# Optimization experiments

Hardware: AMD Instinct MI355X
Metric: run time of the kernel (lower is better)

Reference implementation:

```python
import jax, jax.numpy as jnp
import numpy as np

EPS = 1e-5


def reference(hidden_states, mu_x, W_x1, W_x2, x_bias, W_r, W_k, W_v, W_g,
              A_w, B_w, b_w, bonus, gn_weight, gn_bias, W_o):
    B, T, D = hidden_states.shape
    Hh = bonus.shape[0]
    x = hidden_states
    # token shift: delta = shifted(x) - x, shifted pads one zero row at t=0
    shifted = jnp.pad(x, ((0, 0), (1, 0), (0, 0)))[:, :T]
    delta = shifted - x
    # x_proj: LerpLinear(D -> 5*lr) -> tanh -> einsum with second weight viewed [D,5,lr]
    lr = W_x1.shape[0] // 5
    z = jnp.tanh((x + delta * mu_x) @ W_x1.T).reshape(B, T, 5, lr)
    mus = jnp.einsum('blnr,dnr->blnd', z, W_x2.reshape(D, 5, lr)) + x_bias  # [B,T,5,D]
    r_mu, w_mu, k_mu, v_mu, g_mu = (mus[:, :, i] for i in range(5))
    # DDLerpLinear projections: linear(x + delta * mu)
    r = (x + delta * r_mu) @ W_r.T                                 # [B,T,KD]
    w = jnp.tanh((x + delta * w_mu) @ A_w.T) @ B_w.T + b_w          # LoRA w/ tanh
    k = (x + delta * k_mu) @ W_k.T
    v = (x + delta * v_mu) @ W_v.T                                 # [B,T,VD]
    g = (x + delta * g_mu) @ W_g.T
    K = W_r.shape[0] // Hh
    V = W_v.shape[0] // Hh
    r = r.reshape(B, T, Hh, K)
    k = k.reshape(B, T, Hh, K)
    w = -jnp.exp(w.reshape(B, T, Hh, K))  # log-decay, in (-inf, 0)
    v = v.reshape(B, T, Hh, V)
    u = bonus                              # [Hh, K]

    def step(S, inp):
        q_t, k_t, v_t, w_t = inp           # [B,Hh,K],[B,Hh,K],[B,Hh,V],[B,Hh,K]
        kv = k_t[..., :, None] * v_t[..., None, :]                  # [B,Hh,K,V]
        o_t = jnp.einsum('bhk,bhkv->bhv', q_t, S + u[None, :, :, None] * kv)
        S = jnp.exp(w_t)[..., None] * S + kv
        return S, o_t

    S0 = jnp.zeros((B, Hh, K, V), dtype=x.dtype)
    xs = (jnp.swapaxes(r, 0, 1), jnp.swapaxes(k, 0, 1),
          jnp.swapaxes(v, 0, 1), jnp.swapaxes(w, 0, 1))
    _, o = jax.lax.scan(step, S0, xs)       # o: [T,B,Hh,V]
    o = jnp.swapaxes(o, 0, 1)               # [B,T,Hh,V]
    # GroupNorm(num_heads, value_dim): normalize each head's V channels per token
    mean = o.mean(-1, keepdims=True)
    var = o.var(-1, keepdims=True)
    o = (o - mean) / jnp.sqrt(var + EPS)
    o = o.reshape(B, T, Hh * V) * gn_weight + gn_bias
    o = o * jax.nn.silu(g)                  # swish gate
    return o @ W_o.T


def setup_inputs() -> dict:
    key = jax.random.key(0)
    ks = jax.random.split(key, 16)
    B, T, D = 8, 2048, 1024
    Hh, KD, VD, LR, GLR = 4, 512, 1024, 32, 64
    s = 0.02
    w = lambda k, shape: jax.random.normal(k, shape, jnp.float32) * s
    return {
        'hidden_states': jax.random.normal(ks[0], (B, T, D), jnp.float32),
        'mu_x': w(ks[1], (D,)),
        'W_x1': w(ks[2], (5 * LR, D)),
        'W_x2': w(ks[3], (D, 5 * LR)),
        'x_bias': jnp.zeros((5, D), jnp.float32),
        'W_r': w(ks[4], (KD, D)),
        'W_k': w(ks[5], (KD, D)),
        'W_v': w(ks[6], (VD, D)),
        'W_g': w(ks[7], (VD, D)),
        'A_w': w(ks[8], (GLR, D)),
        'B_w': w(ks[9], (KD, GLR)),
        'b_w': jnp.zeros((KD,), jnp.float32),
        'bonus': w(ks[10], (Hh, KD // Hh)),
        'gn_weight': jnp.ones((VD,), jnp.float32),
        'gn_bias': jnp.zeros((VD,), jnp.float32),
        'W_o': w(ks[11], (D, VD)),
    }
```

## Files before the change

kernel.cpp:

```cpp
#include <hip/hip_runtime.h>
#include <hip/hip_bf16.h>
#include <hip/hip_fp16.h>
#include <cstdint>


typedef _Float16 half8 __attribute__((ext_vector_type(8)));
typedef float f32x4 __attribute__((ext_vector_type(4)));

#define CL 256
#define NP (CL / 2)
#define NC 8

__device__ __forceinline__ float hbits2f(unsigned short us) {
    __half h; *reinterpret_cast<unsigned short*>(&h) = us; return __half2float(h);
}
__device__ __forceinline__ unsigned short f2h(float f) {
    __half h = __float2half(f);
    return *reinterpret_cast<unsigned short*>(&h);
}
__device__ __forceinline__ float2 up2(unsigned int u) {
    return make_float2(hbits2f((unsigned short)(u & 0xFFFF)),
                       hbits2f((unsigned short)(u >> 16)));
}
__device__ __forceinline__ void gload_lds16(const void* g, void* l) {
    __builtin_amdgcn_global_load_lds(
        (const __attribute__((address_space(1))) unsigned*)g,
        (__attribute__((address_space(3))) unsigned*)l, 16, 0, 0);
}

__global__ void cast16(const float* __restrict__ src, __half* __restrict__ dst, int n4)
{
    const int i = blockIdx.x * blockDim.x + threadIdx.x;
    if (i >= n4) return;
    const float4 f = *(const float4*)(src + (size_t)i * 4);
    ushort4 u;
    u.x = f2h(f.x); u.y = f2h(f.y); u.z = f2h(f.z); u.w = f2h(f.w);
    *(ushort4*)(dst + (size_t)i * 4) = u;
}

__global__ void k_xw_h(const float* __restrict__ X, const float* __restrict__ mu,
                       __half* __restrict__ XW, int M, int T)
{
    const size_t i4 = (size_t)blockIdx.x * blockDim.x + threadIdx.x;
    if (i4 >= (size_t)M * 256) return;
    const size_t idx = i4 * 4;
    const int m = (int)(idx >> 10);
    const int d = (int)(idx & 1023);
    const int t = m & (T - 1);
    const float4 xv = *(const float4*)(X + idx);
    const float4 m4 = *(const float4*)(mu + d);
    float4 xp = make_float4(0.f, 0.f, 0.f, 0.f);
    if (t > 0) xp = *(const float4*)(X + idx - 1024);
    ushort4 o;
    o.x = f2h(xv.x + (xp.x - xv.x) * m4.x);
    o.y = f2h(xv.y + (xp.y - xv.y) * m4.y);
    o.z = f2h(xv.z + (xp.z - xv.z) * m4.z);
    o.w = f2h(xv.w + (xp.w - xv.w) * m4.w);
    *(ushort4*)(XW + idx) = o;
}

__global__ __launch_bounds__(256) void gemm16(
    const __half* __restrict__ A, int lda,
    const __half* __restrict__ B, int ldb,
    void* __restrict__ Cv, int ldc,
    int M, int N, int K,
    const float* __restrict__ bias, int epi,
    const float* __restrict__ X, int T)
{
    __shared__ __align__(16) _Float16 As[128 * 32];
    __shared__ __align__(16) _Float16 Bs[128 * 32];

    const int tid = threadIdx.x;

    const int nwg = gridDim.x * gridDim.y;
    int p = blockIdx.y * gridDim.x + blockIdx.x;
    if (!(nwg & 7)) p = (p & 7) * (nwg >> 3) + (p >> 3);
    const int bx = p % gridDim.x, by = p / gridDim.x;

    const int m0 = by * 128;
    const int n0 = bx * 128;
    const int wave = tid >> 6, lane = tid & 63;
    const int wm = wave >> 1, wn = wave & 1;
    const int lr = lane & 15, lk = lane >> 4;

    const int srow = tid >> 2;
    const int scol = (tid & 3) * 8;
    const int arow0 = m0 + srow, arow1 = m0 + 64 + srow;
    int brow0 = n0 + srow;      if (brow0 >= N) brow0 = N - 1;
    int brow1 = n0 + 64 + srow; if (brow1 >= N) brow1 = N - 1;
    char* dA = (char*)As + tid * 16;
    char* dB = (char*)Bs + tid * 16;

    f32x4 acc[4][4] = {};

    for (int k0 = 0; k0 < K; k0 += 32) {
        const __half* gA0 = A + (size_t)arow0 * lda + k0 + scol;
        const __half* gA1 = A + (size_t)arow1 * lda + k0 + scol;
        const __half* gB0 = B + (size_t)brow0 * ldb + k0 + scol;
        const __half* gB1 = B + (size_t)brow1 * ldb + k0 + scol;
        __syncthreads();
        gload_lds16(gA0, dA);
        gload_lds16(gA1, dA + 4096);
        gload_lds16(gB0, dB);
        gload_lds16(gB1, dB + 4096);
        __syncthreads();

        half8 af[4], bf[4];
#pragma unroll
        for (int f = 0; f < 4; f++) {
            af[f] = *(const half8*)&As[(wm * 64 + f * 16 + lr) * 32 + lk * 8];
            bf[f] = *(const half8*)&Bs[(wn * 64 + f * 16 + lr) * 32 + lk * 8];
        }
#pragma unroll
        for (int fm = 0; fm < 4; fm++)
#pragma unroll
            for (int fn = 0; fn < 4; fn++)
                acc[fm][fn] = __builtin_amdgcn_mfma_f32_16x16x32_f16(
                    af[fm], bf[fn], acc[fm][fn], 0, 0, 0);
    }

#pragma unroll
    for (int fm = 0; fm < 4; fm++) {
#pragma unroll
        for (int fn = 0; fn < 4; fn++) {
#pragma unroll
            for (int j = 0; j < 4; j++) {
                const int gm = m0 + wm * 64 + fm * 16 + lk * 4 + j;
                const int gn = n0 + wn * 64 + fn * 16 + lr;
                if (gn >= N) continue;
                float a = acc[fm][fn][j];
                if (epi == 1) {
                    a = tanhf(a);
                    ((__half*)Cv)[(size_t)gm * ldc + gn] = __float2half(a);
                } else if (epi == 2) {
                    a += bias[gn];
                    const float xv = X[(size_t)gm * 1024 + gn];
                    float xp = 0.f;
                    if (gm & (T - 1)) xp = X[(size_t)(gm - 1) * 1024 + gn];
                    ((__half*)Cv)[(size_t)gm * ldc + gn] =
                        __float2half(xv + (xp - xv) * a);
                } else if (epi == 3) {
                    a += bias[gn];
                    ((__half*)Cv)[(size_t)gm * ldc + gn] = __float2half(a);
                } else if (epi == 4) {
                    ((float*)Cv)[(size_t)gm * ldc + gn] = a;
                } else {
                    ((__half*)Cv)[(size_t)gm * ldc + gn] = __float2half(a);
                }
            }
        }
    }
}

__global__ __launch_bounds__(256) void k_prep(
    const __half* __restrict__ R, const __half* __restrict__ Kk,
    const __half* __restrict__ W, const float* __restrict__ bonus,
    unsigned* __restrict__ Eu, float* __restrict__ RU, int T)
{
    const int tok = blockIdx.x;
    const int b = tok >> 11, t = tok & 2047;
    const int h = threadIdx.x >> 6, lane = threadIdx.x & 63;
    const size_t base = (size_t)tok * 512 + h * 128 + 2 * lane;
    const unsigned rr = *(const unsigned*)(R + base);
    const unsigned kk = *(const unsigned*)(Kk + base);
    const unsigned ww = *(const unsigned*)(W + base);
    const float2 rf = up2(rr), kf = up2(kk), wf = up2(ww);
    const float d0 = __expf(-__expf(wf.x));
    const float d1 = __expf(-__expf(wf.y));
    const float2 uf = *(const float2*)(bonus + h * 128 + 2 * lane);
    float ru = rf.x * uf.x * kf.x + rf.y * uf.y * kf.y;
#pragma unroll
    for (int off = 1; off < 64; off <<= 1) ru += __shfl_xor(ru, off);
    const int bh = b * 4 + h;
    unsigned* ep = Eu + (size_t)(bh * T + t) * 192;
    uint2 rkw;
    rkw.x = (rr & 0xFFFFu) | (kk << 16);
    rkw.y = (rr >> 16) | (kk & 0xFFFF0000u);
    *(uint2*)(ep + 2 * lane) = rkw;
    ep[128 + lane] = (unsigned)f2h(d0) | ((unsigned)f2h(d1) << 16);
    if (lane == 0) RU[(size_t)bh * T + t] = ru;
}

__global__ __launch_bounds__(128) void a_gen(
    const unsigned* __restrict__ Eu, __half* __restrict__ Ab,
    float* __restrict__ Abuf, int T)
{
    const int p = blockIdx.x;
    const int l = (p & 7) * 28 + (p >> 3);
    const int bh = l / 7, ci = l - bh * 7;
    const int c = ci + 1;
    const int k = threadIdx.x;
    const int t0 = c * CL;
    const unsigned* ep = Eu + (size_t)(bh * T + t0) * 192;
    __half* ap = Ab + ((size_t)bh * T + t0) * 128 + k;
    const int sel = (k & 1) * 16;
    float D = 1.f;
#pragma unroll 4
    for (int t = 0; t < CL; ++t) {
        const unsigned* e = ep + (size_t)t * 192;
        const unsigned rk = e[k];
        const unsigned dw = e[128 + (k >> 1)];
        const float r = hbits2f((unsigned short)(rk & 0xFFFF));
        const float d = hbits2f((unsigned short)((dw >> sel) & 0xFFFF));
        ap[(size_t)t * 128] = __float2half(r * D);
        D *= d;
    }
    if (c < NC - 1) Abuf[(size_t)(c * 32 + bh) * 128 + k] = D;
}

__global__ __launch_bounds__(256) void rwkv_scan(
    const uint4* __restrict__ E, const __half* __restrict__ V,
    const float* __restrict__ RU, __half* __restrict__ Cout,
    __half* __restrict__ O, int T)
{
    __shared__ uint4 sE[4][96];
    __shared__ uint4 sV[4][16];
    __shared__ float sRU[4][2];

    const int p = blockIdx.x;
    const int l = (p & 7) * 128 + (p >> 3);
    const int bh = l >> 5, c = (l >> 2) & 7, vq = l & 3;
    const int b = bh >> 2, h = bh & 3;
    const int tid = threadIdx.x;
    const int w = tid >> 6, lane = tid & 63;
    const int kg = tid & 15, vg = tid >> 4;
    const int t0 = c * CL;

    const uint4* Eg = E + (size_t)(bh * T + t0) * 48;
    const uint4* Vgp = (const uint4*)(V + ((size_t)b * T + t0) * 1024 + h * 256 + vq * 64);
    const float* RUp = RU + (size_t)bh * T + t0;
    __half* Op = O + ((size_t)b * T + t0) * 1024 + h * 256 + vq * 64 + vg * 4;

    float S[32];
#pragma unroll
    for (int j = 0; j < 32; j++) S[j] = 0.f;

    const int i0 = (kg * 2) ^ ((kg * 2) >> 3);
    const int i1 = (kg * 2 + 1) ^ ((kg * 2 + 1) >> 3);

#define ISSUE(BE, BV, BR, PP)                                                 \
    if (w < 2 && (PP) < NP) {                                                 \
        const int tt = (PP) * 2 + w;                                          \
        if (lane < 48)      BE = Eg[(size_t)tt * 48 + lane];                  \
        else if (lane < 56) BV = Vgp[(size_t)tt * 128 + (lane - 48)];         \
        if (lane == 56)     BR = RUp[tt];                                     \
    }

#define STAGE(BE, BV, BR, SLOT)                                               \
    if (w < 2) {                                                              \
        if (lane < 32)      sE[SLOT][w * 48 + (lane ^ (lane >> 3))] = BE;     \
        else if (lane < 48) sE[SLOT][w * 48 + lane] = BE;                     \
        else if (lane < 56) sV[SLOT][w * 8 + (lane - 48)] = BV;               \
        if (lane == 56)     sRU[SLOT][w] = BR;                                \
    }

#define BAR() do {                                                            \
        asm volatile("s_waitcnt lgkmcnt(0)" ::: "memory");                    \
        __builtin_amdgcn_s_barrier();                                         \
        __builtin_amdgcn_sched_barrier(0);                                    \
    } while (0)

#define COMPUTE(SLOT, SUB, TT)                                                \
    {                                                                         \
        const uint4 rka = sE[SLOT][(SUB) * 48 + i0];                          \
        const uint4 rkb = sE[SLOT][(SUB) * 48 + i1];                          \
        const uint4 dq  = sE[SLOT][(SUB) * 48 + 32 + kg];                     \
        const uint2 vw  = *(const uint2*)((const unsigned*)&sV[SLOT][(SUB) * 8] + vg * 2); \
        const unsigned rw_[8] = {rka.x, rka.y, rka.z, rka.w,                  \
                                 rkb.x, rkb.y, rkb.z, rkb.w};                 \
        const unsigned dw_[4] = {dq.x, dq.y, dq.z, dq.w};                     \
        float r_[8], k_[8], d_[8], vv_[4];                                    \
        _Pragma("unroll") for (int j = 0; j < 8; j++) {                       \
            const float2 rk = up2(rw_[j]); r_[j] = rk.x; k_[j] = rk.y;        \
        }                                                                     \
        _Pragma("unroll") for (int j = 0; j < 4; j++) {                       \
            const float2 dd = up2(dw_[j]); d_[2 * j] = dd.x; d_[2 * j + 1] = dd.y; \
        }                                                                     \
        { const float2 va = up2(vw.x), vb = up2(vw.y);                        \
          vv_[0] = va.x; vv_[1] = va.y; vv_[2] = vb.x; vv_[3] = vb.y; }       \
        float osum[4] = {0.f, 0.f, 0.f, 0.f};                                 \
        _Pragma("unroll") for (int kk = 0; kk < 8; kk++) {                    \
            _Pragma("unroll") for (int vi = 0; vi < 4; vi++) {                \
                osum[vi] = fmaf(r_[kk], S[kk * 4 + vi], osum[vi]);            \
                S[kk * 4 + vi] = fmaf(d_[kk], S[kk * 4 + vi], k_[kk] * vv_[vi]); \
            }                                                                 \
        }                                                                     \
        _Pragma("unroll") for (int vi = 0; vi < 4; vi++) {                    \
            osum[vi] += __shfl_xor(osum[vi], 1);                              \
            osum[vi] += __shfl_xor(osum[vi], 2);                              \
            osum[vi] += __shfl_xor(osum[vi], 4);                              \
            osum[vi] += __shfl_xor(osum[vi], 8);                              \
        }                                                                     \
        if (kg == 0) {                                                        \
            const float ru_ = sRU[SLOT][SUB];                                 \
            ushort4 ou;                                                       \
            ou.x = f2h(osum[0] + ru_ * vv_[0]);                               \
            ou.y = f2h(osum[1] + ru_ * vv_[1]);                               \
            ou.z = f2h(osum[2] + ru_ * vv_[2]);                               \
            ou.w = f2h(osum[3] + ru_ * vv_[3]);                               \
            *(ushort4*)(Op + (size_t)(TT) * 1024) = ou;                       \
        }                                                                     \
    }

#define COMPUTE2(SLOT, PP)  COMPUTE(SLOT, 0, (PP) * 2) COMPUTE(SLOT, 1, (PP) * 2 + 1)

    uint4 e0 = {}, e1 = {}, e2 = {}, e3 = {};
    uint4 v0 = {}, v1 = {}, v2 = {}, v3 = {};
    float r0 = 0.f, r1 = 0.f, r2 = 0.f, r3 = 0.f;

    ISSUE(e0, v0, r0, 0)
    ISSUE(e1, v1, r1, 1)
    ISSUE(e2, v2, r2, 2)
    ISSUE(e3, v3, r3, 3)
    STAGE(e0, v0, r0, 0)
    BAR();

    for (int ps = 0; ps < NP; ps += 4) {
        STAGE(e1, v1, r1, 1)
        ISSUE(e0, v0, r0, ps + 4)
        COMPUTE2(0, ps)
        BAR();
        STAGE(e2, v2, r2, 2)
        ISSUE(e1, v1, r1, ps + 5)
        COMPUTE2(1, ps + 1)
        BAR();
        STAGE(e3, v3, r3, 3)
        ISSUE(e2, v2, r2, ps + 6)
        COMPUTE2(2, ps + 2)
        BAR();
        if (ps + 4 < NP) STAGE(e0, v0, r0, 0)
        ISSUE(e3, v3, r3, ps + 7)
        COMPUTE2(3, ps + 3)
        BAR();
    }

    if (c < NC - 1) {
        __half* Cw = Cout + ((size_t)c * 32 + bh) * 32768 +
                     (size_t)(vq * 64 + vg * 4) * 128 + kg * 8;
#pragma unroll
        for (int vi = 0; vi < 4; vi++) {
            unsigned su[4];
#pragma unroll
            for (int j = 0; j < 4; j++)
                su[j] = (unsigned)f2h(S[(2 * j) * 4 + vi]) |
                        ((unsigned)f2h(S[(2 * j + 1) * 4 + vi]) << 16);
            uint4 s4; s4.x = su[0]; s4.y = su[1]; s4.z = su[2]; s4.w = su[3];
            *(uint4*)(Cw + (size_t)vi * 128) = s4;
        }
    }
#undef ISSUE
#undef STAGE
#undef BAR
#undef COMPUTE
#undef COMPUTE2
}

__global__ __launch_bounds__(256) void rwkv_comb(
    __half* __restrict__ C, const float* __restrict__ A)
{
    const int gid = blockIdx.x * 256 + threadIdx.x;
    const int bh = gid >> 15;
    const int elem = gid & 32767;
    const int k = elem & 127;
    float s = hbits2f(*(const unsigned short*)(C + (size_t)bh * 32768 + elem));
#pragma unroll
    for (int c = 1; c < NC - 1; ++c) {
        const float a = A[(size_t)(c * 32 + bh) * 128 + k];
        __half* cp = C + ((size_t)c * 32 + bh) * 32768 + elem;
        s = a * s + hbits2f(*(const unsigned short*)cp);
        *(unsigned short*)cp = f2h(s);
    }
}

__global__ __launch_bounds__(256) void corr_gemm(
    const __half* __restrict__ Abig, const __half* __restrict__ Cbuf,
    __half* __restrict__ O, int T)
{
    __shared__ __align__(16) _Float16 As[128 * 32];
    __shared__ __align__(16) _Float16 Bs[128 * 32];

    const int tid = threadIdx.x;
    const int p = blockIdx.x;
    const int l = (p & 7) * 112 + (p >> 3);
    const int bhc = l >> 2, mt = (l >> 1) & 1, nt = l & 1;
    const int bh = bhc / 7, ci = bhc - bh * 7;
    const int b = bh >> 2, h = bh & 3;
    const int t0 = (ci + 1) * CL + mt * 128;

    const __half* Ag = Abig + ((size_t)bh * T + t0) * 128;
    const __half* Bg = Cbuf + ((size_t)ci * 32 + bh) * 32768 + (size_t)nt * 128 * 128;
    __half* Og = O + ((size_t)b * T + t0) * 1024 + h * 256 + nt * 128;

    const int wave = tid >> 6, lane = tid & 63;
    const int wm = wave >> 1, wn = wave & 1;
    const int lr = lane & 15, lk = lane >> 4;
    const int srow = tid >> 2;
    const int scol = (tid & 3) * 8;
    char* dA = (char*)As + tid * 16;
    char* dB = (char*)Bs + tid * 16;

    f32x4 acc[4][4] = {};

    for (int k0 = 0; k0 < 128; k0 += 32) {
        const __half* gA0 = Ag + (size_t)srow * 128 + k0 + scol;
        const __half* gA1 = Ag + (size_t)(64 + srow) * 128 + k0 + scol;
        const __half* gB0 = Bg + (size_t)srow * 128 + k0 + scol;
        const __half* gB1 = Bg + (size_t)(64 + srow) * 128 + k0 + scol;
        __syncthreads();
        gload_lds16(gA0, dA);
        gload_lds16(gA1, dA + 4096);
        gload_lds16(gB0, dB);
        gload_lds16(gB1, dB + 4096);
        __syncthreads();

        half8 af[4], bf[4];
#pragma unroll
        for (int f = 0; f < 4; f++) {
            af[f] = *(const half8*)&As[(wm * 64 + f * 16 + lr) * 32 + lk * 8];
            bf[f] = *(const half8*)&Bs[(wn * 64 + f * 16 + lr) * 32 + lk * 8];
        }
#pragma unroll
        for (int fm = 0; fm < 4; fm++)
#pragma unroll
            for (int fn = 0; fn < 4; fn++)
                acc[fm][fn] = __builtin_amdgcn_mfma_f32_16x16x32_f16(
                    af[fm], bf[fn], acc[fm][fn], 0, 0, 0);
    }

#pragma unroll
    for (int fm = 0; fm < 4; fm++) {
#pragma unroll
        for (int fn = 0; fn < 4; fn++) {
#pragma unroll
            for (int j = 0; j < 4; j++) {
                const int row = wm * 64 + fm * 16 + lk * 4 + j;
                const int col = wn * 64 + fn * 16 + lr;
                __half* op = Og + (size_t)row * 1024 + col;
                *op = __float2half(__half2float(*op) + acc[fm][fn][j]);
            }
        }
    }
}

__global__ __launch_bounds__(256) void gn_gate(
    const __half* __restrict__ Obuf, const __half* __restrict__ G,
    const float* __restrict__ gnw, const float* __restrict__ gnb,
    __half* __restrict__ Y)
{
    const int token = blockIdx.x;
    const int wave = threadIdx.x >> 6, lane = threadIdx.x & 63;
    const size_t base = (size_t)token * 1024 + wave * 256 + lane * 4;
    const ushort4 xu = *(const ushort4*)(Obuf + base);
    const float x0 = hbits2f(xu.x), x1 = hbits2f(xu.y),
                x2 = hbits2f(xu.z), x3 = hbits2f(xu.w);
    float sum = x0 + x1 + x2 + x3;
    float ssq = x0 * x0 + x1 * x1 + x2 * x2 + x3 * x3;
#pragma unroll
    for (int off = 32; off >= 1; off >>= 1) {
        sum += __shfl_xor(sum, off);
        ssq += __shfl_xor(ssq, off);
    }
    const float mean = sum * (1.f / 256.f);
    const float var = ssq * (1.f / 256.f) - mean * mean;
    const float rstd = rsqrtf(var + 1e-5f);
    const int c0 = wave * 256 + lane * 4;
    const float4 w4 = *(const float4*)(gnw + c0);
    const float4 b4 = *(const float4*)(gnb + c0);
    const ushort4 gu = *(const ushort4*)(G + base);
    const float g0 = hbits2f(gu.x), g1 = hbits2f(gu.y),
                g2 = hbits2f(gu.z), g3 = hbits2f(gu.w);
    ushort4 y;
    y.x = f2h(((x0 - mean) * rstd * w4.x + b4.x) * (g0 / (1.f + __expf(-g0))));
    y.y = f2h(((x1 - mean) * rstd * w4.y + b4.y) * (g1 / (1.f + __expf(-g1))));
    y.z = f2h(((x2 - mean) * rstd * w4.z + b4.z) * (g2 / (1.f + __expf(-g2))));
    y.w = f2h(((x3 - mean) * rstd * w4.w + b4.w) * (g3 / (1.f + __expf(-g3))));
    *(ushort4*)(Y + base) = y;
}

extern "C" void kernel_launch(void* const* d_in, const int* in_sizes, int n_in,
                              void* d_out, int out_size, void* d_ws, size_t ws_size,
                              hipStream_t stream)
{
    (void)in_sizes; (void)n_in; (void)out_size; (void)ws_size;
    const float* x      = (const float*)d_in[0];
    const float* mu_x   = (const float*)d_in[1];
    const float* W_x1   = (const float*)d_in[2];
    const float* W_x2   = (const float*)d_in[3];
    const float* x_bias = (const float*)d_in[4];
    const float* W_r    = (const float*)d_in[5];
    const float* W_k    = (const float*)d_in[6];
    const float* W_v    = (const float*)d_in[7];
    const float* W_g    = (const float*)d_in[8];
    const float* A_w    = (const float*)d_in[9];
    const float* B_w    = (const float*)d_in[10];
    const float* b_w    = (const float*)d_in[11];
    const float* bonus  = (const float*)d_in[12];
    const float* gnw    = (const float*)d_in[13];
    const float* gnb    = (const float*)d_in[14];
    const float* W_o    = (const float*)d_in[15];

    const int B = 8, T = 2048, M = B * T;

    __half* xwh  = (__half*)d_out;
    __half* inbh = xwh + (size_t)M * 1024;
    __half* Abig = (__half*)((char*)d_out + (size_t)48 * 1024 * 1024);

    __half* z   = (__half*)d_ws;
    __half* w1  = z   + (size_t)M * 160;
    __half* rs  = w1  + (size_t)M * 64;
    __half* ks  = rs  + (size_t)M * 512;
    __half* wsm = ks  + (size_t)M * 512;
    __half* vs  = wsm + (size_t)M * 512;
    __half* gs  = vs  + (size_t)M * 1024;
    float*  ru  = (float*)(gs + (size_t)M * 1024);
    __half* wgt = (__half*)(ru + (size_t)32 * T);
    __half* oh  = rs;
    __half* yb  = wsm;
    __half* Cbuf = wsm;
    float*  Abuf = (float*)z;

    __half* W_x1h = wgt;
    __half* W_x2h = W_x1h + 163840;
    __half* W_rh  = W_x2h + 163840;
    __half* W_kh  = W_rh + 524288;
    __half* W_vh  = W_kh + 524288;
    __half* W_gh  = W_vh + 1048576;
    __half* A_wh  = W_gh + 1048576;
    __half* B_wh  = A_wh + 65536;
    __half* W_oh  = B_wh + 32768;

    const dim3 blk(256);
    auto cgrid = [](int n) { return dim3((n / 4 + 255) / 256); };
    cast16<<<cgrid(163840), blk, 0, stream>>>(W_x1, W_x1h, 163840 / 4);
    cast16<<<cgrid(163840), blk, 0, stream>>>(W_x2, W_x2h, 163840 / 4);
    cast16<<<cgrid(524288), blk, 0, stream>>>(W_r, W_rh, 524288 / 4);
    cast16<<<cgrid(524288), blk, 0, stream>>>(W_k, W_kh, 524288 / 4);
    cast16<<<cgrid(1048576), blk, 0, stream>>>(W_v, W_vh, 1048576 / 4);
    cast16<<<cgrid(1048576), blk, 0, stream>>>(W_g, W_gh, 1048576 / 4);
    cast16<<<cgrid(65536), blk, 0, stream>>>(A_w, A_wh, 65536 / 4);
    cast16<<<cgrid(32768), blk, 0, stream>>>(B_w, B_wh, 32768 / 4);
    cast16<<<cgrid(1048576), blk, 0, stream>>>(W_o, W_oh, 1048576 / 4);

    k_xw_h<<<(M * 256 + 255) / 256, blk, 0, stream>>>(x, mu_x, xwh, M, T);

    auto ggrid = [&](int N) { return dim3((N + 127) / 128, M / 128); };

    gemm16<<<ggrid(160), blk, 0, stream>>>(xwh, 1024, W_x1h, 1024, z, 160,
                                           M, 160, 1024, nullptr, 1, nullptr, T);

    for (int n = 0; n < 5; ++n) {
        gemm16<<<ggrid(1024), blk, 0, stream>>>(z + n * 32, 160, W_x2h + n * 32, 160,
                                                inbh, 1024, M, 1024, 32,
                                                x_bias + n * 1024, 2, x, T);
        if (n == 1) {
            gemm16<<<ggrid(64), blk, 0, stream>>>(inbh, 1024, A_wh, 1024, w1, 64,
                                                  M, 64, 1024, nullptr, 1, nullptr, T);
            gemm16<<<ggrid(512), blk, 0, stream>>>(w1, 64, B_wh, 64, wsm, 512,
                                                   M, 512, 64, b_w, 3, nullptr, T);
        } else {
            __half* Cp = (n == 0) ? rs : (n == 2) ? ks : (n == 3) ? vs : gs;
            const __half* Wp = (n == 0) ? W_rh : (n == 2) ? W_kh : (n == 3) ? W_vh : W_gh;
            const int N = (n == 0 || n == 2) ? 512 : 1024;
            gemm16<<<ggrid(N), blk, 0, stream>>>(inbh, 1024, Wp, 1024, Cp, N,
                                                 M, N, 1024, nullptr, 0, nullptr, T);
        }
    }

    k_prep<<<dim3(M), blk, 0, stream>>>(rs, ks, wsm, bonus,
                                        (unsigned*)d_out, ru, T);

    a_gen<<<dim3(224), dim3(128), 0, stream>>>((const unsigned*)d_out, Abig,
                                               Abuf, T);

    rwkv_scan<<<dim3(1024), blk, 0, stream>>>(
        (const uint4*)d_out, vs, ru, Cbuf, oh, T);
    rwkv_comb<<<dim3(4096), blk, 0, stream>>>(Cbuf, Abuf);
    corr_gemm<<<dim3(896), blk, 0, stream>>>(Abig, Cbuf, oh, T);

    gn_gate<<<dim3(M), blk, 0, stream>>>(oh, gs, gnw, gnb, yb);

    gemm16<<<ggrid(1024), blk, 0, stream>>>(yb, 1024, W_oh, 1024, d_out, 1024,
                                            M, 1024, 1024, nullptr, 4, nullptr, T);
}
```

Baseline: 1.106 ms.

## Merge weight casts into one kernel and read fp16 x in the lerp epilogue

Replaces nine weight-cast launches with a single kernel that indexes into all source buffers, cutting launch overhead. Adds a cast of x to fp16, written into the now-unused xwh buffer after the first GEMM, so the five epi=2 GEMM epilogues read half-width x. The epilogue also carries the previous row's x value across the four rows a lane owns, so only one extra x load per fragment is needed instead of two per element. The trade-off is an extra full pass over x and rounding x to fp16 before the lerp.

```diff
diff --git a/kernel.cpp b/kernel.cpp
--- a/kernel.cpp
+++ b/kernel.cpp
@@ -28,14 +28,38 @@
         (__attribute__((address_space(3))) unsigned*)l, 16, 0, 0);
 }
 
-__global__ void cast16(const float* __restrict__ src, __half* __restrict__ dst, int n4)
-{
-    const int i = blockIdx.x * blockDim.x + threadIdx.x;
-    if (i >= n4) return;
-    const float4 f = *(const float4*)(src + (size_t)i * 4);
+__global__ __launch_bounds__(256) void cast_all(
+    const float* __restrict__ p0, const float* __restrict__ p1,
+    const float* __restrict__ p2, const float* __restrict__ p3,
+    const float* __restrict__ p4, const float* __restrict__ p5,
+    const float* __restrict__ p6, const float* __restrict__ p7,
+    const float* __restrict__ p8, __half* __restrict__ dst)
+{
+    const int v = blockIdx.x * 256 + threadIdx.x;
+    const float* s; int off;
+    if      (v < 40960)  { s = p0; off = v; }
+    else if (v < 81920)  { s = p1; off = v - 40960; }
+    else if (v < 212992) { s = p2; off = v - 81920; }
+    else if (v < 344064) { s = p3; off = v - 212992; }
+    else if (v < 606208) { s = p4; off = v - 344064; }
+    else if (v < 868352) { s = p5; off = v - 606208; }
+    else if (v < 884736) { s = p6; off = v - 868352; }
+    else if (v < 892928) { s = p7; off = v - 884736; }
+    else                 { s = p8; off = v - 892928; }
+    const float4 f = *(const float4*)(s + (size_t)off * 4);
     ushort4 u;
     u.x = f2h(f.x); u.y = f2h(f.y); u.z = f2h(f.z); u.w = f2h(f.w);
-    *(ushort4*)(dst + (size_t)i * 4) = u;
+    *(ushort4*)(dst + (size_t)v * 4) = u;
+}
+
+__global__ __launch_bounds__(256) void cast_x(const float* __restrict__ x,
+                                              __half* __restrict__ xh)
+{
+    const size_t v = (size_t)blockIdx.x * 256 + threadIdx.x;
+    const float4 f = *(const float4*)(x + v * 4);
+    ushort4 u;
+    u.x = f2h(f.x); u.y = f2h(f.y); u.z = f2h(f.z); u.w = f2h(f.w);
+    *(ushort4*)(xh + v * 4) = u;
 }
 
 __global__ void k_xw_h(const float* __restrict__ X, const float* __restrict__ mu,
@@ -65,7 +89,7 @@
     void* __restrict__ Cv, int ldc,
     int M, int N, int K,
     const float* __restrict__ bias, int epi,
-    const float* __restrict__ X, int T)
+    const __half* __restrict__ X, int T)
 {
     __shared__ __align__(16) _Float16 As[128 * 32];
     __shared__ __align__(16) _Float16 Bs[128 * 32];
@@ -123,22 +147,25 @@
     for (int fm = 0; fm < 4; fm++) {
 #pragma unroll
         for (int fn = 0; fn < 4; fn++) {
+            const int gm0 = m0 + wm * 64 + fm * 16 + lk * 4;
+            const int gn = n0 + wn * 64 + fn * 16 + lr;
+            if (gn >= N) continue;
+            float xprev = 0.f;
+            if (epi == 2 && (gm0 & (T - 1)))
+                xprev = __half2float(X[(size_t)(gm0 - 1) * 1024 + gn]);
 #pragma unroll
             for (int j = 0; j < 4; j++) {
-                const int gm = m0 + wm * 64 + fm * 16 + lk * 4 + j;
-                const int gn = n0 + wn * 64 + fn * 16 + lr;
-                if (gn >= N) continue;
+                const int gm = gm0 + j;
                 float a = acc[fm][fn][j];
                 if (epi == 1) {
                     a = tanhf(a);
                     ((__half*)Cv)[(size_t)gm * ldc + gn] = __float2half(a);
                 } else if (epi == 2) {
                     a += bias[gn];
-                    const float xv = X[(size_t)gm * 1024 + gn];
-                    float xp = 0.f;
-                    if (gm & (T - 1)) xp = X[(size_t)(gm - 1) * 1024 + gn];
+                    const float xv = __half2float(X[(size_t)gm * 1024 + gn]);
                     ((__half*)Cv)[(size_t)gm * ldc + gn] =
-                        __float2half(xv + (xp - xv) * a);
+                        __float2half(xv + (xprev - xv) * a);
+                    xprev = xv;
                 } else if (epi == 3) {
                     a += bias[gn];
                     ((__half*)Cv)[(size_t)gm * ldc + gn] = __float2half(a);
@@ -503,6 +530,7 @@
 
     __half* xwh  = (__half*)d_out;
     __half* inbh = xwh + (size_t)M * 1024;
+    __half* xh   = xwh;
     __half* Abig = (__half*)((char*)d_out + (size_t)48 * 1024 * 1024);
 
     __half* z   = (__half*)d_ws;
@@ -530,16 +558,8 @@
     __half* W_oh  = B_wh + 32768;
 
     const dim3 blk(256);
-    auto cgrid = [](int n) { return dim3((n / 4 + 255) / 256); };
-    cast16<<<cgrid(163840), blk, 0, stream>>>(W_x1, W_x1h, 163840 / 4);
-    cast16<<<cgrid(163840), blk, 0, stream>>>(W_x2, W_x2h, 163840 / 4);
-    cast16<<<cgrid(524288), blk, 0, stream>>>(W_r, W_rh, 524288 / 4);
-    cast16<<<cgrid(524288), blk, 0, stream>>>(W_k, W_kh, 524288 / 4);
-    cast16<<<cgrid(1048576), blk, 0, stream>>>(W_v, W_vh, 1048576 / 4);
-    cast16<<<cgrid(1048576), blk, 0, stream>>>(W_g, W_gh, 1048576 / 4);
-    cast16<<<cgrid(65536), blk, 0, stream>>>(A_w, A_wh, 65536 / 4);
-    cast16<<<cgrid(32768), blk, 0, stream>>>(B_w, B_wh, 32768 / 4);
-    cast16<<<cgrid(1048576), blk, 0, stream>>>(W_o, W_oh, 1048576 / 4);
+    cast_all<<<dim3(4512), blk, 0, stream>>>(W_x1, W_x2, W_r, W_k, W_v, W_g,
+                                             A_w, B_w, W_o, wgt);
 
     k_xw_h<<<(M * 256 + 255) / 256, blk, 0, stream>>>(x, mu_x, xwh, M, T);
 
@@ -547,11 +567,13 @@
 
     gemm16<<<ggrid(160), blk, 0, stream>>>(xwh, 1024, W_x1h, 1024, z, 160,
                                            M, 160, 1024, nullptr, 1, nullptr, T);
+
+    cast_x<<<dim3(16384), blk, 0, stream>>>(x, xh);
 
     for (int n = 0; n < 5; ++n) {
         gemm16<<<ggrid(1024), blk, 0, stream>>>(z + n * 32, 160, W_x2h + n * 32, 160,
                                                 inbh, 1024, M, 1024, 32,
-                                                x_bias + n * 1024, 2, x, T);
+                                                x_bias + n * 1024, 2, xh, T);
         if (n == 1) {
             gemm16<<<ggrid(64), blk, 0, stream>>>(inbh, 1024, A_wh, 1024, w1, 64,
                                                   M, 64, 1024, nullptr, 1, nullptr, T);
```

Result: faster. 1.071 ms (-3.2%).
